# Performance work log

Measured on AMD Instinct MI355X. Metric: run time of the kernel, lower is better.

The kernel has to match this reference:

```python
import jax, jax.numpy as jnp
import numpy as np

BN_EPS = 1e-5
N_IN, N_OUT, K, CIN, COUT = 2_000_000, 250_000, 8, 32, 64


def setup_inputs() -> dict:
    key = jax.random.key(0)
    k1, k2, k3 = jax.random.split(key, 3)
    x = jax.random.normal(k1, (N_IN, CIN), dtype=jnp.float32)
    neigh = jax.random.randint(k2, (N_OUT, K), 0, N_IN, dtype=jnp.int64)
    weight = jax.random.normal(k3, (K, CIN, COUT), dtype=jnp.float32) * 0.05
    gamma = jnp.ones((COUT,), dtype=jnp.float32)
    beta = jnp.zeros((COUT,), dtype=jnp.float32)
    return {"x": x, "neigh": neigh, "weight": weight, "gamma": gamma, "beta": beta}


def reference(x, neigh, weight, gamma, beta):
    # Octree conv (nempty=True, stride 2): gather K child-octant features, GEMM.
    gathered = x[neigh]                      # [N_out, K, Cin]
    out = jnp.einsum('nkc,kcd->nd', gathered, weight)  # [N_out, Cout]
    # BatchNorm1d (training mode: batch statistics over octants)
    mean = jnp.mean(out, axis=0)
    var = jnp.var(out, axis=0)
    y = (out - mean) * jax.lax.rsqrt(var + BN_EPS) * gamma + beta
    return y
```

## Files before the change

### kernel.cpp

```cpp
#include <hip/hip_runtime.h>
#include <hip/hip_bf16.h>

#define N_OUT_ROWS 250000
#define TILES 15625
#define NBLK 512
#define WPB 4
#define NWAVES (NBLK * WPB)
#define BN_EPS 1e-5f

typedef __attribute__((ext_vector_type(8))) short bf16x8;
typedef __attribute__((ext_vector_type(8))) unsigned short u16x8;
typedef __attribute__((ext_vector_type(4))) float f32x4;

static __device__ __forceinline__ unsigned short f2bf(float f) {
  union { float f; unsigned u; } v; v.f = f;
  unsigned r = v.u + 0x7FFFu + ((v.u >> 16) & 1u);
  return (unsigned short)(r >> 16);
}
static __device__ __forceinline__ float bf2f(unsigned short s) {
  union { unsigned u; float f; } v; v.u = ((unsigned)s) << 16;
  return v.f;
}

#define GLOAD_LDS16(gsrc, ldst)                                                \
  __builtin_amdgcn_global_load_lds(                                            \
      (const __attribute__((address_space(1))) unsigned int*)(gsrc),           \
      (__attribute__((address_space(3))) unsigned int*)(ldst), 16, 0, 0)

__global__ void k_prep(const float* __restrict__ w,
                       unsigned short* __restrict__ bfrag,
                       float* __restrict__ stats) {
  const int i = blockIdx.x * 256 + threadIdx.x;
  if (i < 128) stats[i] = 0.f;
  const int f = i >> 6, l = i & 63;
  const int kt = f >> 2, ct = f & 3, rr = l & 15, gg = l >> 4;
  u16x8 o;
  #pragma unroll
  for (int j = 0; j < 8; ++j)
    o[j] = f2bf(w[(kt * 32 + gg * 8 + j) * 64 + ct * 16 + rr]);
  *reinterpret_cast<u16x8*>(bfrag + i * 8) = o;
}

template <bool BF16OUT>
__global__ __launch_bounds__(256, 2)
void k_gemm(const float* __restrict__ x, const int* __restrict__ neigh,
            const unsigned short* __restrict__ bfrag,
            float* __restrict__ outf, unsigned short* __restrict__ outb,
            float* __restrict__ stats) {
  __shared__ __align__(16) unsigned char Abuf_all[WPB][16384];
  __shared__ float wpart[WPB][128];

  const int tid = threadIdx.x;
  const int lane = tid & 63;
  const int widx = tid >> 6;
  unsigned char* Abuf = Abuf_all[widx];

  bf16x8 bf[8][4];
  #pragma unroll
  for (int kt = 0; kt < 8; ++kt)
    #pragma unroll
    for (int ct = 0; ct < 4; ++ct)
      bf[kt][ct] = *reinterpret_cast<const bf16x8*>(
          bfrag + ((kt * 4 + ct) * 64 + lane) * 8);

  const int gw = blockIdx.x * WPB + widx;
  const int q = TILES / NWAVES;
  const int rem = TILES % NWAVES;
  const int start = (gw < rem) ? gw * (q + 1) : rem * (q + 1) + (gw - rem) * q;
  const int cnt = q + (gw < rem ? 1 : 0);

  const int r = lane & 15;
  const int g4 = lane >> 4;
  const int seg = lane & 7;
  const int ktl = lane >> 3;
  const int swz = (r & 7) << 4;
  const int rdbase = (r << 10) + (g4 << 5);

  float sacc[4] = {0.f, 0.f, 0.f, 0.f};
  float qacc[4] = {0.f, 0.f, 0.f, 0.f};

  for (int k = 0; k < cnt; ++k) {
    const int t = start + k;
    const int n0 = t << 4;

    int idxv[16];
    #pragma unroll
    for (int m = 0; m < 16; ++m)
      idxv[m] = neigh[(n0 + m) * 8 + ktl];

    asm volatile("s_waitcnt lgkmcnt(0)" ::: "memory");
    __builtin_amdgcn_sched_barrier(0);

    #pragma unroll
    for (int j = 0; j < 16; ++j) {
      const float* src = x + (size_t)idxv[j] * 32 + ((seg ^ (j & 7)) << 2);
      GLOAD_LDS16(src, Abuf + j * 1024);
    }

    asm volatile("s_waitcnt vmcnt(0)" ::: "memory");
    __builtin_amdgcn_sched_barrier(0);

    f32x4 acc[4];
    #pragma unroll
    for (int ct = 0; ct < 4; ++ct) acc[ct] = (f32x4){0.f, 0.f, 0.f, 0.f};

    #pragma unroll
    for (int kt = 0; kt < 8; ++kt) {
      const int o0 = rdbase + (kt << 7);
      const f32x4 a0 = *reinterpret_cast<const f32x4*>(Abuf + (o0 ^ swz));
      const f32x4 a1 = *reinterpret_cast<const f32x4*>(Abuf + ((o0 + 16) ^ swz));
      union { bf16x8 v; __hip_bfloat162 h[4]; } af;
      af.h[0] = __float22bfloat162_rn(make_float2(a0[0], a0[1]));
      af.h[1] = __float22bfloat162_rn(make_float2(a0[2], a0[3]));
      af.h[2] = __float22bfloat162_rn(make_float2(a1[0], a1[1]));
      af.h[3] = __float22bfloat162_rn(make_float2(a1[2], a1[3]));
      #pragma unroll
      for (int ct = 0; ct < 4; ++ct)
        acc[ct] = __builtin_amdgcn_mfma_f32_16x16x32_bf16(af.v, bf[kt][ct],
                                                          acc[ct], 0, 0, 0);
    }

    const int rbase = n0 + g4 * 4;
    #pragma unroll
    for (int ct = 0; ct < 4; ++ct) {
      #pragma unroll
      for (int j = 0; j < 4; ++j) {
        const int off = (rbase + j) * 64 + ct * 16 + r;
        if (BF16OUT) outb[off] = f2bf(acc[ct][j]);
        else         outf[off] = acc[ct][j];
      }
      sacc[ct] += acc[ct][0] + acc[ct][1] + acc[ct][2] + acc[ct][3];
      qacc[ct] += acc[ct][0] * acc[ct][0] + acc[ct][1] * acc[ct][1] +
                  acc[ct][2] * acc[ct][2] + acc[ct][3] * acc[ct][3];
    }
  }

  #pragma unroll
  for (int ct = 0; ct < 4; ++ct) {
    sacc[ct] += __shfl_xor(sacc[ct], 16);
    qacc[ct] += __shfl_xor(qacc[ct], 16);
    sacc[ct] += __shfl_xor(sacc[ct], 32);
    qacc[ct] += __shfl_xor(qacc[ct], 32);
  }
  if (lane < 16) {
    #pragma unroll
    for (int ct = 0; ct < 4; ++ct) {
      wpart[widx][ct * 16 + lane] = sacc[ct];
      wpart[widx][64 + ct * 16 + lane] = qacc[ct];
    }
  }
  __syncthreads();
  if (tid < 128) {
    atomicAdd(&stats[tid], wpart[0][tid] + wpart[1][tid] +
                           wpart[2][tid] + wpart[3][tid]);
  }
}

template <bool BF16IN>
__global__ __launch_bounds__(256)
void k_bn(float* __restrict__ out, const unsigned short* __restrict__ inb,
          const float* __restrict__ stats, const float* __restrict__ gamma,
          const float* __restrict__ beta) {
  __shared__ float sc[64], bs[64];
  if (threadIdx.x < 64) {
    const int d = threadIdx.x;
    const float inv = 1.0f / (float)N_OUT_ROWS;
    const float mean = stats[d] * inv;
    const float var = stats[64 + d] * inv - mean * mean;
    const float rstd = rsqrtf(var + BN_EPS);
    const float scale = rstd * gamma[d];
    sc[d] = scale;
    bs[d] = beta[d] - mean * scale;
  }
  __syncthreads();

  if (BF16IN) {
    const int total8 = N_OUT_ROWS * 64 / 8;
    for (int i = blockIdx.x * blockDim.x + threadIdx.x; i < total8;
         i += gridDim.x * blockDim.x) {
      const int d0 = (i & 7) << 3;
      const u16x8 v = *reinterpret_cast<const u16x8*>(inb + i * 8);
      float4 o0, o1;
      o0.x = bf2f(v[0]) * sc[d0 + 0] + bs[d0 + 0];
      o0.y = bf2f(v[1]) * sc[d0 + 1] + bs[d0 + 1];
      o0.z = bf2f(v[2]) * sc[d0 + 2] + bs[d0 + 2];
      o0.w = bf2f(v[3]) * sc[d0 + 3] + bs[d0 + 3];
      o1.x = bf2f(v[4]) * sc[d0 + 4] + bs[d0 + 4];
      o1.y = bf2f(v[5]) * sc[d0 + 5] + bs[d0 + 5];
      o1.z = bf2f(v[6]) * sc[d0 + 6] + bs[d0 + 6];
      o1.w = bf2f(v[7]) * sc[d0 + 7] + bs[d0 + 7];
      reinterpret_cast<float4*>(out)[i * 2] = o0;
      reinterpret_cast<float4*>(out)[i * 2 + 1] = o1;
    }
  } else {
    const int total4 = N_OUT_ROWS * 64 / 4;
    float4* o4 = reinterpret_cast<float4*>(out);
    for (int i = blockIdx.x * blockDim.x + threadIdx.x; i < total4;
         i += gridDim.x * blockDim.x) {
      const int d0 = (i & 15) << 2;
      float4 v = o4[i];
      v.x = v.x * sc[d0]     + bs[d0];
      v.y = v.y * sc[d0 + 1] + bs[d0 + 1];
      v.z = v.z * sc[d0 + 2] + bs[d0 + 2];
      v.w = v.w * sc[d0 + 3] + bs[d0 + 3];
      o4[i] = v;
    }
  }
}

extern "C" void kernel_launch(void* const* d_in, const int* in_sizes, int n_in,
                              void* d_out, int out_size, void* d_ws, size_t ws_size,
                              hipStream_t stream) {
  const float* x     = (const float*)d_in[0];
  const int*   neigh = (const int*)d_in[1];
  const float* w     = (const float*)d_in[2];
  const float* gamma = (const float*)d_in[3];
  const float* beta  = (const float*)d_in[4];
  float* out = (float*)d_out;

  float* stats = (float*)d_ws;
  unsigned short* bfrag = (unsigned short*)((char*)d_ws + 1024);
  unsigned short* obf = (unsigned short*)((char*)d_ws + 65536);

  const bool bf16path =
      ws_size >= (size_t)65536 + (size_t)N_OUT_ROWS * 64 * 2;

  k_prep<<<8, 256, 0, stream>>>(w, bfrag, stats);
  if (bf16path) {
    k_gemm<true><<<NBLK, 256, 0, stream>>>(x, neigh, bfrag, nullptr, obf, stats);
    k_bn<true><<<2048, 256, 0, stream>>>(out, obf, stats, gamma, beta);
  } else {
    k_gemm<false><<<NBLK, 256, 0, stream>>>(x, neigh, bfrag, out, nullptr, stats);
    k_bn<false><<<2048, 256, 0, stream>>>(out, nullptr, stats, gamma, beta);
  }
}
```

Measured before the change: 80.36 us.

## Fuse gather-GEMM and BatchNorm into one kernel with grid-wide barrier

Merges the GEMM+stats kernel and the BN apply kernel into a single persistent launch. An atomic grid barrier waits for all stats to be accumulated, then each block normalizes the bf16 tiles it wrote itself, which are likely still in L2. This removes one kernel launch and the cold re-read of the intermediate. The cost is a memset plus a spin barrier that assumes all 512 blocks are co-resident, and it risks deadlock if occupancy falls below that.

```diff
diff --git a/kernel.cpp b/kernel.cpp
--- a/kernel.cpp
+++ b/kernel.cpp
@@ -27,11 +27,15 @@
       (const __attribute__((address_space(1))) unsigned int*)(gsrc),           \
       (__attribute__((address_space(3))) unsigned int*)(ldst), 16, 0, 0)
 
+static __device__ __forceinline__ int tile_start(int g) {
+  const int q = TILES / NWAVES;
+  const int rem = TILES % NWAVES;
+  return (g < rem) ? g * (q + 1) : rem * (q + 1) + (g - rem) * q;
+}
+
 __global__ void k_prep(const float* __restrict__ w,
-                       unsigned short* __restrict__ bfrag,
-                       float* __restrict__ stats) {
+                       unsigned short* __restrict__ bfrag) {
   const int i = blockIdx.x * 256 + threadIdx.x;
-  if (i < 128) stats[i] = 0.f;
   const int f = i >> 6, l = i & 63;
   const int kt = f >> 2, ct = f & 3, rr = l & 15, gg = l >> 4;
   u16x8 o;
@@ -41,14 +45,15 @@
   *reinterpret_cast<u16x8*>(bfrag + i * 8) = o;
 }
 
-template <bool BF16OUT>
 __global__ __launch_bounds__(256, 2)
-void k_gemm(const float* __restrict__ x, const int* __restrict__ neigh,
-            const unsigned short* __restrict__ bfrag,
-            float* __restrict__ outf, unsigned short* __restrict__ outb,
-            float* __restrict__ stats) {
+void k_fused(const float* __restrict__ x, const int* __restrict__ neigh,
+             const unsigned short* __restrict__ bfrag,
+             unsigned short* __restrict__ obf, float* __restrict__ out,
+             float* __restrict__ stats, unsigned int* __restrict__ bar,
+             const float* __restrict__ gamma, const float* __restrict__ beta) {
   __shared__ __align__(16) unsigned char Abuf_all[WPB][16384];
   __shared__ float wpart[WPB][128];
+  __shared__ float sc[64], bs[64];
 
   const int tid = threadIdx.x;
   const int lane = tid & 63;
@@ -64,10 +69,8 @@
           bfrag + ((kt * 4 + ct) * 64 + lane) * 8);
 
   const int gw = blockIdx.x * WPB + widx;
-  const int q = TILES / NWAVES;
-  const int rem = TILES % NWAVES;
-  const int start = (gw < rem) ? gw * (q + 1) : rem * (q + 1) + (gw - rem) * q;
-  const int cnt = q + (gw < rem ? 1 : 0);
+  const int start = tile_start(gw);
+  const int cnt = tile_start(gw + 1) - start;
 
   const int r = lane & 15;
   const int g4 = lane >> 4;
@@ -124,11 +127,8 @@
     #pragma unroll
     for (int ct = 0; ct < 4; ++ct) {
       #pragma unroll
-      for (int j = 0; j < 4; ++j) {
-        const int off = (rbase + j) * 64 + ct * 16 + r;
-        if (BF16OUT) outb[off] = f2bf(acc[ct][j]);
-        else         outf[off] = acc[ct][j];
-      }
+      for (int j = 0; j < 4; ++j)
+        obf[(rbase + j) * 64 + ct * 16 + r] = f2bf(acc[ct][j]);
       sacc[ct] += acc[ct][0] + acc[ct][1] + acc[ct][2] + acc[ct][3];
       qacc[ct] += acc[ct][0] * acc[ct][0] + acc[ct][1] * acc[ct][1] +
                   acc[ct][2] * acc[ct][2] + acc[ct][3] * acc[ct][3];
@@ -154,57 +154,165 @@
     atomicAdd(&stats[tid], wpart[0][tid] + wpart[1][tid] +
                            wpart[2][tid] + wpart[3][tid]);
   }
-}
-
-template <bool BF16IN>
+
+  __syncthreads();
+  if (tid == 0) {
+    __threadfence();
+    __hip_atomic_fetch_add(bar, 1u, __ATOMIC_ACQ_REL, __HIP_MEMORY_SCOPE_AGENT);
+    unsigned v;
+    do {
+      v = __hip_atomic_load(bar, __ATOMIC_ACQUIRE, __HIP_MEMORY_SCOPE_AGENT);
+      if (v < NBLK) __builtin_amdgcn_s_sleep(32);
+    } while (v < NBLK);
+  }
+  __syncthreads();
+
+  if (tid < 64) {
+    const float inv = 1.0f / (float)N_OUT_ROWS;
+    const float sum = __hip_atomic_load(&stats[tid], __ATOMIC_RELAXED,
+                                        __HIP_MEMORY_SCOPE_AGENT);
+    const float ssq = __hip_atomic_load(&stats[64 + tid], __ATOMIC_RELAXED,
+                                        __HIP_MEMORY_SCOPE_AGENT);
+    const float mean = sum * inv;
+    const float var = ssq * inv - mean * mean;
+    const float scale = rsqrtf(var + BN_EPS) * gamma[tid];
+    sc[tid] = scale;
+    bs[tid] = beta[tid] - mean * scale;
+  }
+  __syncthreads();
+
+  const int bt0 = tile_start(blockIdx.x * WPB);
+  const int bt1 = tile_start(blockIdx.x * WPB + WPB);
+  const int nchunk = (bt1 - bt0) * 128;
+  const int base = bt0 * 128;
+  for (int i = tid; i < nchunk; i += 256) {
+    const int c = base + i;
+    const u16x8 v = *reinterpret_cast<const u16x8*>(obf + (size_t)c * 8);
+    const int d0 = (c & 7) << 3;
+    float4 o0, o1;
+    o0.x = bf2f(v[0]) * sc[d0 + 0] + bs[d0 + 0];
+    o0.y = bf2f(v[1]) * sc[d0 + 1] + bs[d0 + 1];
+    o0.z = bf2f(v[2]) * sc[d0 + 2] + bs[d0 + 2];
+    o0.w = bf2f(v[3]) * sc[d0 + 3] + bs[d0 + 3];
+    o1.x = bf2f(v[4]) * sc[d0 + 4] + bs[d0 + 4];
+    o1.y = bf2f(v[5]) * sc[d0 + 5] + bs[d0 + 5];
+    o1.z = bf2f(v[6]) * sc[d0 + 6] + bs[d0 + 6];
+    o1.w = bf2f(v[7]) * sc[d0 + 7] + bs[d0 + 7];
+    reinterpret_cast<float4*>(out)[c * 2] = o0;
+    reinterpret_cast<float4*>(out)[c * 2 + 1] = o1;
+  }
+}
+
+__global__ __launch_bounds__(256, 2)
+void k_gemm_f32(const float* __restrict__ x, const int* __restrict__ neigh,
+                const unsigned short* __restrict__ bfrag,
+                float* __restrict__ outf, float* __restrict__ stats) {
+  __shared__ __align__(16) unsigned char Abuf_all[WPB][16384];
+  __shared__ float wpart[WPB][128];
+  const int tid = threadIdx.x;
+  const int lane = tid & 63;
+  const int widx = tid >> 6;
+  unsigned char* Abuf = Abuf_all[widx];
+  bf16x8 bf[8][4];
+  #pragma unroll
+  for (int kt = 0; kt < 8; ++kt)
+    #pragma unroll
+    for (int ct = 0; ct < 4; ++ct)
+      bf[kt][ct] = *reinterpret_cast<const bf16x8*>(
+          bfrag + ((kt * 4 + ct) * 64 + lane) * 8);
+  const int gw = blockIdx.x * WPB + widx;
+  const int start = tile_start(gw), cnt = tile_start(gw + 1) - start;
+  const int r = lane & 15, g4 = lane >> 4, seg = lane & 7, ktl = lane >> 3;
+  const int swz = (r & 7) << 4, rdbase = (r << 10) + (g4 << 5);
+  float sacc[4] = {0,0,0,0}, qacc[4] = {0,0,0,0};
+  for (int k = 0; k < cnt; ++k) {
+    const int n0 = (start + k) << 4;
+    int idxv[16];
+    #pragma unroll
+    for (int m = 0; m < 16; ++m) idxv[m] = neigh[(n0 + m) * 8 + ktl];
+    asm volatile("s_waitcnt lgkmcnt(0)" ::: "memory");
+    __builtin_amdgcn_sched_barrier(0);
+    #pragma unroll
+    for (int j = 0; j < 16; ++j) {
+      const float* src = x + (size_t)idxv[j] * 32 + ((seg ^ (j & 7)) << 2);
+      GLOAD_LDS16(src, Abuf + j * 1024);
+    }
+    asm volatile("s_waitcnt vmcnt(0)" ::: "memory");
+    __builtin_amdgcn_sched_barrier(0);
+    f32x4 acc[4];
+    #pragma unroll
+    for (int ct = 0; ct < 4; ++ct) acc[ct] = (f32x4){0,0,0,0};
+    #pragma unroll
+    for (int kt = 0; kt < 8; ++kt) {
+      const int o0 = rdbase + (kt << 7);
+      const f32x4 a0 = *reinterpret_cast<const f32x4*>(Abuf + (o0 ^ swz));
+      const f32x4 a1 = *reinterpret_cast<const f32x4*>(Abuf + ((o0 + 16) ^ swz));
+      union { bf16x8 v; __hip_bfloat162 h[4]; } af;
+      af.h[0] = __float22bfloat162_rn(make_float2(a0[0], a0[1]));
+      af.h[1] = __float22bfloat162_rn(make_float2(a0[2], a0[3]));
+      af.h[2] = __float22bfloat162_rn(make_float2(a1[0], a1[1]));
+      af.h[3] = __float22bfloat162_rn(make_float2(a1[2], a1[3]));
+      #pragma unroll
+      for (int ct = 0; ct < 4; ++ct)
+        acc[ct] = __builtin_amdgcn_mfma_f32_16x16x32_bf16(af.v, bf[kt][ct],
+                                                          acc[ct], 0, 0, 0);
+    }
+    const int rbase = n0 + g4 * 4;
+    #pragma unroll
+    for (int ct = 0; ct < 4; ++ct) {
+      #pragma unroll
+      for (int j = 0; j < 4; ++j)
+        outf[(rbase + j) * 64 + ct * 16 + r] = acc[ct][j];
+      sacc[ct] += acc[ct][0] + acc[ct][1] + acc[ct][2] + acc[ct][3];
+      qacc[ct] += acc[ct][0] * acc[ct][0] + acc[ct][1] * acc[ct][1] +
+                  acc[ct][2] * acc[ct][2] + acc[ct][3] * acc[ct][3];
+    }
+  }
+  #pragma unroll
+  for (int ct = 0; ct < 4; ++ct) {
+    sacc[ct] += __shfl_xor(sacc[ct], 16);
+    qacc[ct] += __shfl_xor(qacc[ct], 16);
+    sacc[ct] += __shfl_xor(sacc[ct], 32);
+    qacc[ct] += __shfl_xor(qacc[ct], 32);
+  }
+  if (lane < 16) {
+    #pragma unroll
+    for (int ct = 0; ct < 4; ++ct) {
+      wpart[widx][ct * 16 + lane] = sacc[ct];
+      wpart[widx][64 + ct * 16 + lane] = qacc[ct];
+    }
+  }
+  __syncthreads();
+  if (tid < 128)
+    atomicAdd(&stats[tid], wpart[0][tid] + wpart[1][tid] +
+                           wpart[2][tid] + wpart[3][tid]);
+}
+
 __global__ __launch_bounds__(256)
-void k_bn(float* __restrict__ out, const unsigned short* __restrict__ inb,
-          const float* __restrict__ stats, const float* __restrict__ gamma,
-          const float* __restrict__ beta) {
+void k_bn_f32(float* __restrict__ out, const float* __restrict__ stats,
+              const float* __restrict__ gamma, const float* __restrict__ beta) {
   __shared__ float sc[64], bs[64];
   if (threadIdx.x < 64) {
     const int d = threadIdx.x;
     const float inv = 1.0f / (float)N_OUT_ROWS;
     const float mean = stats[d] * inv;
     const float var = stats[64 + d] * inv - mean * mean;
-    const float rstd = rsqrtf(var + BN_EPS);
-    const float scale = rstd * gamma[d];
+    const float scale = rsqrtf(var + BN_EPS) * gamma[d];
     sc[d] = scale;
     bs[d] = beta[d] - mean * scale;
   }
   __syncthreads();
-
-  if (BF16IN) {
-    const int total8 = N_OUT_ROWS * 64 / 8;
-    for (int i = blockIdx.x * blockDim.x + threadIdx.x; i < total8;
-         i += gridDim.x * blockDim.x) {
-      const int d0 = (i & 7) << 3;
-      const u16x8 v = *reinterpret_cast<const u16x8*>(inb + i * 8);
-      float4 o0, o1;
-      o0.x = bf2f(v[0]) * sc[d0 + 0] + bs[d0 + 0];
-      o0.y = bf2f(v[1]) * sc[d0 + 1] + bs[d0 + 1];
-      o0.z = bf2f(v[2]) * sc[d0 + 2] + bs[d0 + 2];
-      o0.w = bf2f(v[3]) * sc[d0 + 3] + bs[d0 + 3];
-      o1.x = bf2f(v[4]) * sc[d0 + 4] + bs[d0 + 4];
-      o1.y = bf2f(v[5]) * sc[d0 + 5] + bs[d0 + 5];
-      o1.z = bf2f(v[6]) * sc[d0 + 6] + bs[d0 + 6];
-      o1.w = bf2f(v[7]) * sc[d0 + 7] + bs[d0 + 7];
-      reinterpret_cast<float4*>(out)[i * 2] = o0;
-      reinterpret_cast<float4*>(out)[i * 2 + 1] = o1;
-    }
-  } else {
-    const int total4 = N_OUT_ROWS * 64 / 4;
-    float4* o4 = reinterpret_cast<float4*>(out);
-    for (int i = blockIdx.x * blockDim.x + threadIdx.x; i < total4;
-         i += gridDim.x * blockDim.x) {
-      const int d0 = (i & 15) << 2;
-      float4 v = o4[i];
-      v.x = v.x * sc[d0]     + bs[d0];
-      v.y = v.y * sc[d0 + 1] + bs[d0 + 1];
-      v.z = v.z * sc[d0 + 2] + bs[d0 + 2];
-      v.w = v.w * sc[d0 + 3] + bs[d0 + 3];
-      o4[i] = v;
-    }
+  const int total4 = N_OUT_ROWS * 64 / 4;
+  float4* o4 = reinterpret_cast<float4*>(out);
+  for (int i = blockIdx.x * blockDim.x + threadIdx.x; i < total4;
+       i += gridDim.x * blockDim.x) {
+    const int d0 = (i & 15) << 2;
+    float4 v = o4[i];
+    v.x = v.x * sc[d0]     + bs[d0];
+    v.y = v.y * sc[d0 + 1] + bs[d0 + 1];
+    v.z = v.z * sc[d0 + 2] + bs[d0 + 2];
+    v.w = v.w * sc[d0 + 3] + bs[d0 + 3];
+    o4[i] = v;
   }
 }
 
@@ -219,18 +327,20 @@
   float* out = (float*)d_out;
 
   float* stats = (float*)d_ws;
+  unsigned int* bar = (unsigned int*)((char*)d_ws + 512);
   unsigned short* bfrag = (unsigned short*)((char*)d_ws + 1024);
   unsigned short* obf = (unsigned short*)((char*)d_ws + 65536);
 
-  const bool bf16path =
+  const bool fused =
       ws_size >= (size_t)65536 + (size_t)N_OUT_ROWS * 64 * 2;
 
-  k_prep<<<8, 256, 0, stream>>>(w, bfrag, stats);
-  if (bf16path) {
-    k_gemm<true><<<NBLK, 256, 0, stream>>>(x, neigh, bfrag, nullptr, obf, stats);
-    k_bn<true><<<2048, 256, 0, stream>>>(out, obf, stats, gamma, beta);
+  hipMemsetAsync(d_ws, 0, 1024, stream);
+  k_prep<<<8, 256, 0, stream>>>(w, bfrag);
+  if (fused) {
+    k_fused<<<NBLK, 256, 0, stream>>>(x, neigh, bfrag, obf, out, stats, bar,
+                                      gamma, beta);
   } else {
-    k_gemm<false><<<NBLK, 256, 0, stream>>>(x, neigh, bfrag, out, nullptr, stats);
-    k_bn<false><<<2048, 256, 0, stream>>>(out, nullptr, stats, gamma, beta);
-  }
-}
+    k_gemm_f32<<<NBLK, 256, 0, stream>>>(x, neigh, bfrag, out, stats);
+    k_bn_f32<<<2048, 256, 0, stream>>>(out, stats, gamma, beta);
+  }
+}
```

Measured after the change: 154.3 us. 1.92x slower.

## Split each tile across a wave pair sharing LDS to raise occupancy

Applied to the files above, without the earlier changes.

Pairs of waves now share one 16 KB LDS tile buffer. Each wave gathers half the rows and computes half the output column tiles, so it holds only 2 weight fragments per k-step. This halves per-block LDS and B-fragment registers, which allows 3 blocks per CU and a 768-block grid. The cost is two block-wide __syncthreads per tile iteration, which serialise the gather and compute phases across all waves in the block, and the 8 activation rows are converted to bf16 twice, once per wave.

```diff
diff --git a/kernel.cpp b/kernel.cpp
--- a/kernel.cpp
+++ b/kernel.cpp
@@ -3,10 +3,11 @@
 
 #define N_OUT_ROWS 250000
 #define TILES 15625
-#define NBLK 512
+#define NBLK 768
 #define WPB 4
-#define NWAVES (NBLK * WPB)
 #define BN_EPS 1e-5f
+
+#define SB() __builtin_amdgcn_sched_barrier(0)
 
 typedef __attribute__((ext_vector_type(8))) short bf16x8;
 typedef __attribute__((ext_vector_type(8))) unsigned short u16x8;
@@ -42,32 +43,37 @@
 }
 
 template <bool BF16OUT>
-__global__ __launch_bounds__(256, 2)
+__global__ __launch_bounds__(256, 3)
 void k_gemm(const float* __restrict__ x, const int* __restrict__ neigh,
             const unsigned short* __restrict__ bfrag,
             float* __restrict__ outf, unsigned short* __restrict__ outb,
             float* __restrict__ stats) {
-  __shared__ __align__(16) unsigned char Abuf_all[WPB][16384];
+  __shared__ __align__(16) unsigned char Abuf_all[2][16384];
   __shared__ float wpart[WPB][128];
 
   const int tid = threadIdx.x;
   const int lane = tid & 63;
   const int widx = tid >> 6;
-  unsigned char* Abuf = Abuf_all[widx];
-
-  bf16x8 bf[8][4];
+  const int pairid = widx >> 1;
+  const int half = widx & 1;
+  const int ctg0 = half << 1;
+  unsigned char* Abuf = Abuf_all[pairid];
+
+  bf16x8 bf[8][2];
   #pragma unroll
   for (int kt = 0; kt < 8; ++kt)
     #pragma unroll
-    for (int ct = 0; ct < 4; ++ct)
-      bf[kt][ct] = *reinterpret_cast<const bf16x8*>(
-          bfrag + ((kt * 4 + ct) * 64 + lane) * 8);
-
-  const int gw = blockIdx.x * WPB + widx;
-  const int q = TILES / NWAVES;
-  const int rem = TILES % NWAVES;
-  const int start = (gw < rem) ? gw * (q + 1) : rem * (q + 1) + (gw - rem) * q;
-  const int cnt = q + (gw < rem ? 1 : 0);
+    for (int c = 0; c < 2; ++c)
+      bf[kt][c] = *reinterpret_cast<const bf16x8*>(
+          bfrag + ((kt * 4 + ctg0 + c) * 64 + lane) * 8);
+
+  const int b = blockIdx.x;
+  const int q = TILES / NBLK;
+  const int rem = TILES % NBLK;
+  const int s_b = (b < rem) ? b * (q + 1) : rem * (q + 1) + (b - rem) * q;
+  const int c_b = q + (b < rem ? 1 : 0);
+  const int e_b = s_b + c_b;
+  const int K = (c_b + 1) >> 1;
 
   const int r = lane & 15;
   const int g4 = lane >> 4;
@@ -75,78 +81,89 @@
   const int ktl = lane >> 3;
   const int swz = (r & 7) << 4;
   const int rdbase = (r << 10) + (g4 << 5);
-
-  float sacc[4] = {0.f, 0.f, 0.f, 0.f};
-  float qacc[4] = {0.f, 0.f, 0.f, 0.f};
-
-  for (int k = 0; k < cnt; ++k) {
-    const int t = start + k;
-    const int n0 = t << 4;
-
-    int idxv[16];
+  const int jbase = half << 3;
+
+  float sacc[2] = {0.f, 0.f};
+  float qacc[2] = {0.f, 0.f};
+
+  for (int k2 = 0; k2 < K; ++k2) {
+    const int t = s_b + (k2 << 1) + pairid;
+    const bool active = t < e_b;
+
+    int idxv[8];
+    if (active) {
+      #pragma unroll
+      for (int m = 0; m < 8; ++m)
+        idxv[m] = neigh[((t << 4) + jbase + m) * 8 + ktl];
+    }
+
+    __syncthreads();
+
+    if (active) {
+      SB();
+      #pragma unroll
+      for (int j = 0; j < 8; ++j) {
+        const int ch = jbase + j;
+        const float* src = x + (size_t)idxv[j] * 32 + ((seg ^ (ch & 7)) << 2);
+        GLOAD_LDS16(src, Abuf + ch * 1024);
+      }
+      SB();
+      asm volatile("s_waitcnt vmcnt(0)" ::: "memory");
+    }
+    __syncthreads();
+
+    if (active) {
+      f32x4 acc[2];
+      acc[0] = (f32x4){0.f, 0.f, 0.f, 0.f};
+      acc[1] = (f32x4){0.f, 0.f, 0.f, 0.f};
+
+      #pragma unroll
+      for (int kt = 0; kt < 8; ++kt) {
+        const int o0 = rdbase + (kt << 7);
+        const f32x4 a0 = *reinterpret_cast<const f32x4*>(Abuf + (o0 ^ swz));
+        const f32x4 a1 = *reinterpret_cast<const f32x4*>(Abuf + ((o0 + 16) ^ swz));
+        union { bf16x8 v; __hip_bfloat162 h[4]; } af;
+        af.h[0] = __float22bfloat162_rn(make_float2(a0[0], a0[1]));
+        af.h[1] = __float22bfloat162_rn(make_float2(a0[2], a0[3]));
+        af.h[2] = __float22bfloat162_rn(make_float2(a1[0], a1[1]));
+        af.h[3] = __float22bfloat162_rn(make_float2(a1[2], a1[3]));
+        acc[0] = __builtin_amdgcn_mfma_f32_16x16x32_bf16(af.v, bf[kt][0],
+                                                         acc[0], 0, 0, 0);
+        acc[1] = __builtin_amdgcn_mfma_f32_16x16x32_bf16(af.v, bf[kt][1],
+                                                         acc[1], 0, 0, 0);
+      }
+
+      const int rbase = (t << 4) + g4 * 4;
+      #pragma unroll
+      for (int c = 0; c < 2; ++c) {
+        #pragma unroll
+        for (int j = 0; j < 4; ++j) {
+          const int off = (rbase + j) * 64 + (ctg0 + c) * 16 + r;
+          if (BF16OUT) outb[off] = f2bf(acc[c][j]);
+          else         outf[off] = acc[c][j];
+        }
+        sacc[c] += acc[c][0] + acc[c][1] + acc[c][2] + acc[c][3];
+        qacc[c] += acc[c][0] * acc[c][0] + acc[c][1] * acc[c][1] +
+                   acc[c][2] * acc[c][2] + acc[c][3] * acc[c][3];
+      }
+    }
+  }
+
+  #pragma unroll
+  for (int c = 0; c < 2; ++c) {
+    sacc[c] += __shfl_xor(sacc[c], 16);
+    qacc[c] += __shfl_xor(qacc[c], 16);
+    sacc[c] += __shfl_xor(sacc[c], 32);
+    qacc[c] += __shfl_xor(qacc[c], 32);
+  }
+  if (lane < 16) {
+    const int other = ctg0 ^ 2;
     #pragma unroll
-    for (int m = 0; m < 16; ++m)
-      idxv[m] = neigh[(n0 + m) * 8 + ktl];
-
-    asm volatile("s_waitcnt lgkmcnt(0)" ::: "memory");
-    __builtin_amdgcn_sched_barrier(0);
-
-    #pragma unroll
-    for (int j = 0; j < 16; ++j) {
-      const float* src = x + (size_t)idxv[j] * 32 + ((seg ^ (j & 7)) << 2);
-      GLOAD_LDS16(src, Abuf + j * 1024);
-    }
-
-    asm volatile("s_waitcnt vmcnt(0)" ::: "memory");
-    __builtin_amdgcn_sched_barrier(0);
-
-    f32x4 acc[4];
-    #pragma unroll
-    for (int ct = 0; ct < 4; ++ct) acc[ct] = (f32x4){0.f, 0.f, 0.f, 0.f};
-
-    #pragma unroll
-    for (int kt = 0; kt < 8; ++kt) {
-      const int o0 = rdbase + (kt << 7);
-      const f32x4 a0 = *reinterpret_cast<const f32x4*>(Abuf + (o0 ^ swz));
-      const f32x4 a1 = *reinterpret_cast<const f32x4*>(Abuf + ((o0 + 16) ^ swz));
-      union { bf16x8 v; __hip_bfloat162 h[4]; } af;
-      af.h[0] = __float22bfloat162_rn(make_float2(a0[0], a0[1]));
-      af.h[1] = __float22bfloat162_rn(make_float2(a0[2], a0[3]));
-      af.h[2] = __float22bfloat162_rn(make_float2(a1[0], a1[1]));
-      af.h[3] = __float22bfloat162_rn(make_float2(a1[2], a1[3]));
-      #pragma unroll
-      for (int ct = 0; ct < 4; ++ct)
-        acc[ct] = __builtin_amdgcn_mfma_f32_16x16x32_bf16(af.v, bf[kt][ct],
-                                                          acc[ct], 0, 0, 0);
-    }
-
-    const int rbase = n0 + g4 * 4;
-    #pragma unroll
-    for (int ct = 0; ct < 4; ++ct) {
-      #pragma unroll
-      for (int j = 0; j < 4; ++j) {
-        const int off = (rbase + j) * 64 + ct * 16 + r;
-        if (BF16OUT) outb[off] = f2bf(acc[ct][j]);
-        else         outf[off] = acc[ct][j];
-      }
-      sacc[ct] += acc[ct][0] + acc[ct][1] + acc[ct][2] + acc[ct][3];
-      qacc[ct] += acc[ct][0] * acc[ct][0] + acc[ct][1] * acc[ct][1] +
-                  acc[ct][2] * acc[ct][2] + acc[ct][3] * acc[ct][3];
-    }
-  }
-
-  #pragma unroll
-  for (int ct = 0; ct < 4; ++ct) {
-    sacc[ct] += __shfl_xor(sacc[ct], 16);
-    qacc[ct] += __shfl_xor(qacc[ct], 16);
-    sacc[ct] += __shfl_xor(sacc[ct], 32);
-    qacc[ct] += __shfl_xor(qacc[ct], 32);
-  }
-  if (lane < 16) {
-    #pragma unroll
-    for (int ct = 0; ct < 4; ++ct) {
-      wpart[widx][ct * 16 + lane] = sacc[ct];
-      wpart[widx][64 + ct * 16 + lane] = qacc[ct];
+    for (int c = 0; c < 2; ++c) {
+      wpart[widx][(ctg0 + c) * 16 + lane] = sacc[c];
+      wpart[widx][64 + (ctg0 + c) * 16 + lane] = qacc[c];
+      wpart[widx][(other + c) * 16 + lane] = 0.f;
+      wpart[widx][64 + (other + c) * 16 + lane] = 0.f;
     }
   }
   __syncthreads();
```

Result: slower. 84.37 us (+5.0%).
